# Kernel optimization log

Hardware: AMD Instinct MI355X
Metric: run time of the kernel (lower is better)

The kernel has to match this reference:

```python
import jax, jax.numpy as jnp
import numpy as np

BIG_NUMBER = 1000000.0


def setup_inputs() -> dict:
    key = jax.random.key(0)
    ks = jax.random.split(key, 20)
    B, N, F, MID, OUT = 2, 512, 128, 128, 128
    node_fts = jax.random.normal(ks[0], (B, N, F), jnp.float32)
    edge_fts = jax.random.normal(ks[1], (B, N, N, F), jnp.float32)
    graph_fts = jax.random.normal(ks[2], (B, F), jnp.float32)
    hidden = jax.random.normal(ks[3], (B, N, F), jnp.float32)
    # Bernoulli(0.5) adjacency + self-loops so masked max is always valid
    adj = (jax.random.uniform(ks[4], (B, N, N)) < 0.5).astype(jnp.float32)
    adj = jnp.maximum(adj, jnp.eye(N, dtype=jnp.float32)[None])
    Z = 2 * F  # z = cat(node_fts, hidden)

    def lin(k, fan_in, fan_out):
        kw, kb = jax.random.split(k)
        lim = 1.0 / np.sqrt(fan_in)
        W = jax.random.uniform(kw, (fan_in, fan_out), jnp.float32, -lim, lim)
        b = jax.random.uniform(kb, (fan_out,), jnp.float32, -lim, lim)
        return W, b

    W1, b1 = lin(ks[5], Z, MID)
    W2, b2 = lin(ks[6], Z, MID)
    We, be = lin(ks[7], F, MID)
    Wg, bg = lin(ks[8], F, MID)
    Wo1, bo1 = lin(ks[9], Z, OUT)
    Wo2, bo2 = lin(ks[10], MID, OUT)
    return dict(node_fts=node_fts, edge_fts=edge_fts, graph_fts=graph_fts,
                adj_mat=adj, hidden=hidden,
                W1=W1, b1=b1, W2=W2, b2=b2, We=We, be=be, Wg=Wg, bg=bg,
                Wo1=Wo1, bo1=bo1, Wo2=Wo2, bo2=bo2)


def reference(node_fts, edge_fts, graph_fts, adj_mat, hidden,
              W1, b1, W2, b2, We, be, Wg, bg, Wo1, bo1, Wo2, bo2):
    # z: (B, N, 2F)
    z = jnp.concatenate([node_fts, hidden], axis=-1)
    msg_1 = z @ W1 + b1                      # (B, N, mid) - sender
    msg_2 = z @ W2 + b2                      # (B, N, mid) - receiver
    msg_e = edge_fts @ We + be               # (B, N, N, mid)
    msg_g = graph_fts @ Wg + bg              # (B, mid)
    # msgs[b, i, j] = msg_1[b, j] + msg_2[b, i] + msg_e[b, i, j] + msg_g[b]
    msgs = (msg_1[:, None, :, :] + msg_2[:, :, None, :]
            + msg_e + msg_g[:, None, None, :])  # (B, N, N, mid)
    # masked max over axis 1 (senders in the torch reduction dim=1)
    maxarg = jnp.where(adj_mat[..., None] > 0, msgs, -BIG_NUMBER)
    msgs_red = jnp.max(maxarg, axis=1)       # (B, N, mid)
    h_1 = z @ Wo1 + bo1
    h_2 = msgs_red @ Wo2 + bo2
    ret = jax.nn.relu(h_1 + h_2)             # (B, N, out)
    return ret
```

## Files before the change

### kernel.cpp

```cpp
#include <hip/hip_runtime.h>


typedef __bf16 bf16x8 __attribute__((ext_vector_type(8)));
typedef float  f32x4  __attribute__((ext_vector_type(4)));

#define MFMA16(a,b,c) __builtin_amdgcn_mfma_f32_16x16x32_bf16(a,b,c,0,0,0)

union BFrag { bf16x8 v; unsigned short s[8]; unsigned u[4]; };

__device__ __forceinline__ unsigned packbf(float lo, float hi){
  return __builtin_amdgcn_perm(__builtin_bit_cast(unsigned, hi),
                               __builtin_bit_cast(unsigned, lo), 0x07060302u);
}
__device__ __forceinline__ unsigned short f2bt(float f){
  return (unsigned short)(__builtin_bit_cast(unsigned, f) >> 16);
}
__device__ __forceinline__ unsigned short f2b(float f){
  unsigned u = __builtin_bit_cast(unsigned, f);
  u = u + 0x7FFFu + ((u >> 16) & 1u);
  return (unsigned short)(u >> 16);
}
__device__ __forceinline__ float b2f(unsigned short u){
  unsigned v = ((unsigned)u) << 16;
  return __builtin_bit_cast(float, v);
}

#define WAITVM(N) asm volatile("s_waitcnt vmcnt(" #N ")" ::: "memory")

#define WS_MS2  0
#define WS_MS1  131072
#define WS_H1   262144
#define WS_MSGG 393216
#define WS_PART 393472
#define WS_WEFR 4587776

__global__ __launch_bounds__(64) void k1_small(
    const float* __restrict__ node,
    const float* __restrict__ hidden,
    const float* __restrict__ graph,
    const float* __restrict__ W1, const float* __restrict__ b1,
    const float* __restrict__ W2, const float* __restrict__ b2,
    const float* __restrict__ Wo1,const float* __restrict__ bo1,
    const float* __restrict__ Wg, const float* __restrict__ bg,
    const float* __restrict__ We,
    float* __restrict__ ws)
{
  int bid  = blockIdx.x;
  int lane = threadIdx.x;
  int col = lane & 15, quad = lane >> 4;

  if (bid < 192) {
    int mat = bid >> 6;
    int rt  = bid & 63;
    int r0  = rt * 16;
    const float* W  = (mat==0) ? W1 : (mat==1) ? W2 : Wo1;
    const float* bb = (mat==0) ? b1 : (mat==1) ? b2 : bo1;
    float* dst = ws + ((mat==0) ? WS_MS1 : (mat==1) ? WS_MS2 : WS_H1);

    bf16x8 a[8];
    long rowb = (long)(r0 + col) * 128;
#pragma unroll
    for (int kk = 0; kk < 8; ++kk) {
      const float* src = (kk < 4) ? node : hidden;
      int f = (kk & 3) * 32 + quad * 8;
      f32x4 v0 = *(const f32x4*)(src + rowb + f);
      f32x4 v1 = *(const f32x4*)(src + rowb + f + 4);
      BFrag t;
      t.u[0] = packbf(v0[0], v0[1]); t.u[1] = packbf(v0[2], v0[3]);
      t.u[2] = packbf(v1[0], v1[1]); t.u[3] = packbf(v1[2], v1[3]);
      a[kk] = t.v;
    }
    f32x4 acc[8];
#pragma unroll
    for (int nt = 0; nt < 8; ++nt) acc[nt] = (f32x4)0.f;
#pragma unroll
    for (int kk = 0; kk < 8; ++kk) {
      BFrag bf[8];
#pragma unroll
      for (int nt = 0; nt < 8; ++nt)
#pragma unroll
        for (int j = 0; j < 8; ++j)
          bf[nt].s[j] = f2bt(W[(kk*32 + quad*8 + j)*128 + nt*16 + col]);
#pragma unroll
      for (int nt = 0; nt < 8; ++nt) acc[nt] = MFMA16(a[kk], bf[nt].v, acc[nt]);
    }
#pragma unroll
    for (int nt = 0; nt < 8; ++nt) {
      float bv = bb[nt*16 + col];
#pragma unroll
      for (int r = 0; r < 4; ++r) {
        int row = r0 + quad*4 + r;
        dst[(long)row*128 + nt*16 + col] = acc[nt][r] + bv;
      }
    }
  } else if (bid < 194) {
    int b = bid - 192;
    float a0 = 0.f, a1 = 0.f;
    for (int k = 0; k < 128; ++k) {
      float g = graph[b*128 + k];
      a0 += g * Wg[k*128 + lane];
      a1 += g * Wg[k*128 + 64 + lane];
    }
    ws[WS_MSGG + b*128 + lane]      = a0 + bg[lane];
    ws[WS_MSGG + b*128 + 64 + lane] = a1 + bg[64 + lane];
  } else {
    unsigned short* wf = (unsigned short*)(ws + WS_WEFR);
#pragma unroll
    for (int kk = 0; kk < 4; ++kk)
#pragma unroll
      for (int nt = 0; nt < 8; ++nt) {
        BFrag t;
#pragma unroll
        for (int e = 0; e < 8; ++e)
          t.s[e] = f2b(We[(kk*32 + quad*8 + e)*128 + nt*16 + col]);
        *(bf16x8*)(wf + ((kk*8 + nt)*64 + lane)*8) = t.v;
      }
  }
}

__device__ __forceinline__ void issue_slice(const float* ei, void* lbase, int lane){
  int l5 = lane >> 5, s5 = lane & 31;
#pragma unroll
  for (int inst = 0; inst < 8; ++inst) {
    int j = inst*2 + l5;
    const float* gp = ei + j*128 + ((s5 ^ j) << 2);
    __builtin_amdgcn_global_load_lds(
        (const __attribute__((address_space(1))) void*)gp,
        (__attribute__((address_space(3))) void*)((char*)lbase + inst*1024),
        16, 0, 0);
  }
}

__global__ __launch_bounds__(64, 1) void k2_main(
    const float* __restrict__ E,
    const float* __restrict__ adj,
    const float* __restrict__ msg2,
    const unsigned short* __restrict__ wefrag,
    float* __restrict__ part)
{
  __shared__ alignas(16) unsigned char lds_raw[4*8192 + 4096 + 512];
  unsigned short* const m2l  = (unsigned short*)(lds_raw + 32768);
  unsigned short* const adjl = (unsigned short*)(lds_raw + 32768 + 4096);

  const int bid = blockIdx.x;
  const int jt = bid & 31, s = (bid >> 5) & 31, b = bid >> 10;
  const int lane = threadIdx.x;
  const int col = lane & 15, quad = lane >> 4;
  const int i0 = s * 16, j0 = jt * 16;

  const float* Eb = E + ((long)(b*512 + i0)*512 + j0) * 128;

  bf16x8 bfr[4][8];
#pragma unroll
  for (int kk = 0; kk < 4; ++kk)
#pragma unroll
    for (int nt = 0; nt < 8; ++nt)
      bfr[kk][nt] = *(const bf16x8*)(wefrag + ((kk*8 + nt)*64 + lane)*8);

#pragma unroll
  for (int p = 0; p < 8; ++p) {
    int f = p*256 + lane*4;
    const float* mp = msg2 + (long)(b*512 + i0 + (f >> 7))*128 + (f & 127);
    f32x4 v = *(const f32x4*)mp;
    uint2 uu;
    uu.x = (unsigned)f2b(v[0]) | ((unsigned)f2b(v[1]) << 16);
    uu.y = (unsigned)f2b(v[2]) | ((unsigned)f2b(v[3]) << 16);
    *(uint2*)(m2l + f) = uu;
  }
  {
    int row = lane >> 2, c4 = (lane & 3) * 4;
    f32x4 v = *(const f32x4*)(adj + (long)(b*512 + i0 + row)*512 + j0 + c4);
    uint2 uu;
    uu.x = (unsigned)f2bt(v[0]) | ((unsigned)f2bt(v[1]) << 16);
    uu.y = (unsigned)f2bt(v[2]) | ((unsigned)f2bt(v[3]) << 16);
    *(uint2*)(adjl + row*16 + c4) = uu;
  }
  __syncthreads();

#pragma unroll
  for (int d = 0; d < 4; ++d)
    issue_slice(Eb + (long)d*65536, lds_raw + d*8192, lane);

  f32x4 mx[8];
#pragma unroll
  for (int nt = 0; nt < 8; ++nt) mx[nt] = (f32x4)(-1.0e6f);

  auto body = [&](int ii) {
    const float* sl = (const float*)(lds_raw + (ii & 3) * 8192);
    BFrag a[4];
#pragma unroll
    for (int kk = 0; kk < 4; ++kk) {
      int cb = kk*8 + quad*2;
      f32x4 v0 = *(const f32x4*)(sl + col*128 + ((cb    ) ^ col)*4);
      f32x4 v1 = *(const f32x4*)(sl + col*128 + ((cb + 1) ^ col)*4);
      a[kk].u[0] = packbf(v0[0], v0[1]); a[kk].u[1] = packbf(v0[2], v0[3]);
      a[kk].u[2] = packbf(v1[0], v1[1]); a[kk].u[3] = packbf(v1[2], v1[3]);
    }
    float m2[8];
#pragma unroll
    for (int nt = 0; nt < 8; ++nt) m2[nt] = b2f(m2l[ii*128 + nt*16 + col]);
    ushort4 av = *(const ushort4*)(adjl + ii*16 + quad*4);
    f32x4 biasv;
    biasv[0] = b2f(av.x)*1.0e6f - 1.0e6f;
    biasv[1] = b2f(av.y)*1.0e6f - 1.0e6f;
    biasv[2] = b2f(av.z)*1.0e6f - 1.0e6f;
    biasv[3] = b2f(av.w)*1.0e6f - 1.0e6f;
    f32x4 T[8];
#pragma unroll
    for (int nt = 0; nt < 8; ++nt) T[nt] = biasv + m2[nt];
#pragma unroll
    for (int kk = 0; kk < 4; ++kk)
#pragma unroll
      for (int nt = 0; nt < 8; ++nt)
        T[nt] = MFMA16(a[kk].v, bfr[kk][nt], T[nt]);
#pragma unroll
    for (int nt = 0; nt < 8; ++nt)
#pragma unroll
      for (int r = 0; r < 4; ++r)
        mx[nt][r] = fmaxf(mx[nt][r], T[nt][r]);
  };

#pragma unroll 1
  for (int ii = 0; ii < 12; ++ii) {
    WAITVM(24);
    body(ii);
    asm volatile("" ::: "memory");
    issue_slice(Eb + (long)(ii+4)*65536, lds_raw + (ii & 3)*8192, lane);
  }
  WAITVM(24); body(12);
  WAITVM(16); body(13);
  WAITVM(8);  body(14);
  WAITVM(0);  body(15);

  float* pp = part + ((long)((b*32 + jt)*32 + s)) * 2048;
#pragma unroll
  for (int nt = 0; nt < 8; ++nt)
#pragma unroll
    for (int r = 0; r < 4; ++r)
      pp[(quad*4 + r)*128 + nt*16 + col] = mx[nt][r];
}

__global__ __launch_bounds__(64) void k3_out(
    const float* __restrict__ ws,
    const float* __restrict__ Wo2,
    const float* __restrict__ be,
    const float* __restrict__ bo2,
    float* __restrict__ out)
{
  int bid = blockIdx.x;
  int b = bid >> 5, jt = bid & 31, j0 = jt * 16;
  int lane = threadIdx.x, col = lane & 15, quad = lane >> 4;

  const float* part = ws + WS_PART + ((long)((b*32 + jt)*32))*2048;
  const float* msg1 = ws + WS_MS1;
  const float* msgg = ws + WS_MSGG + b*128;
  const float* h1   = ws + WS_H1;

  BFrag af[4];
#pragma unroll
  for (int kk = 0; kk < 4; ++kk) {
    int off = kk*32 + quad*8;
    const float* p0 = part + col*128 + off;
    f32x4 v0 = *(const f32x4*)(p0);
    f32x4 v1 = *(const f32x4*)(p0 + 4);
#pragma unroll
    for (int s = 1; s < 32; ++s) {
      f32x4 u0 = *(const f32x4*)(p0 + s*2048);
      f32x4 u1 = *(const f32x4*)(p0 + s*2048 + 4);
#pragma unroll
      for (int r = 0; r < 4; ++r) { v0[r] = fmaxf(v0[r], u0[r]); v1[r] = fmaxf(v1[r], u1[r]); }
    }
    const float* m1 = msg1 + (long)(b*512 + j0 + col)*128 + off;
    f32x4 w0 = *(const f32x4*)m1, w1 = *(const f32x4*)(m1 + 4);
#pragma unroll
    for (int r = 0; r < 4; ++r) {
      float g0 = msgg[off + r]     + be[off + r];
      float g1 = msgg[off + 4 + r] + be[off + 4 + r];
      af[kk].s[r]     = f2b(v0[r] + w0[r] + g0);
      af[kk].s[4 + r] = f2b(v1[r] + w1[r] + g1);
    }
  }

  f32x4 acc[8];
#pragma unroll
  for (int nt = 0; nt < 8; ++nt) acc[nt] = (f32x4)0.f;
#pragma unroll
  for (int kk = 0; kk < 4; ++kk) {
    BFrag bf[8];
#pragma unroll
    for (int nt = 0; nt < 8; ++nt)
#pragma unroll
      for (int j = 0; j < 8; ++j)
        bf[nt].s[j] = f2bt(Wo2[(kk*32 + quad*8 + j)*128 + nt*16 + col]);
#pragma unroll
    for (int nt = 0; nt < 8; ++nt) acc[nt] = MFMA16(af[kk].v, bf[nt].v, acc[nt]);
  }

#pragma unroll
  for (int nt = 0; nt < 8; ++nt) {
    float bv = bo2[nt*16 + col];
#pragma unroll
    for (int r = 0; r < 4; ++r) {
      int row = j0 + quad*4 + r;
      long idx = (long)(b*512 + row)*128 + nt*16 + col;
      float v = h1[idx] + acc[nt][r] + bv;
      out[idx] = v < 0.f ? 0.f : v;
    }
  }
}

extern "C" void kernel_launch(void* const* d_in, const int* in_sizes, int n_in,
                              void* d_out, int out_size, void* d_ws, size_t ws_size,
                              hipStream_t stream)
{
  const float* node   = (const float*)d_in[0];
  const float* E      = (const float*)d_in[1];
  const float* graph  = (const float*)d_in[2];
  const float* adj    = (const float*)d_in[3];
  const float* hidden = (const float*)d_in[4];
  const float* W1  = (const float*)d_in[5];
  const float* b1  = (const float*)d_in[6];
  const float* W2  = (const float*)d_in[7];
  const float* b2  = (const float*)d_in[8];
  const float* We  = (const float*)d_in[9];
  const float* be  = (const float*)d_in[10];
  const float* Wg  = (const float*)d_in[11];
  const float* bg  = (const float*)d_in[12];
  const float* Wo1 = (const float*)d_in[13];
  const float* bo1 = (const float*)d_in[14];
  const float* Wo2 = (const float*)d_in[15];
  const float* bo2 = (const float*)d_in[16];
  float* ws  = (float*)d_ws;
  float* out = (float*)d_out;

  hipLaunchKernelGGL(k1_small, dim3(195), dim3(64), 0, stream,
                     node, hidden, graph, W1, b1, W2, b2, Wo1, bo1, Wg, bg, We, ws);
  hipLaunchKernelGGL(k2_main, dim3(2048), dim3(64), 0, stream,
                     E, adj, ws + WS_MS2, (const unsigned short*)(ws + WS_WEFR),
                     ws + WS_PART);
  hipLaunchKernelGGL(k3_out, dim3(64), dim3(64), 0, stream,
                     ws, Wo2, be, bo2, out);
}
```

Measured before the change: 430.7 us.

## Store partial maxima as bf16, shrink edge ring to three slots, vectorize msg2 reads

The main kernel now writes its per-slice partial max results as bf16 rather than fp32, which halves the partial-buffer traffic between k2 and k3. k3 reads these partials with 16-byte bf16 loads. The prefetch ring for edge slices drops from four 8KB LDS slots to three, reducing LDS per block at the cost of less prefetch depth. msg2 is stored transposed in LDS so each lane fetches its eight values with one vector load instead of eight scalar loads. The extra bf16 rounding of the partial maxima may slightly change numerics.

```diff
diff --git a/kernel.cpp b/kernel.cpp
--- a/kernel.cpp
+++ b/kernel.cpp
@@ -136,11 +136,11 @@
     const float* __restrict__ adj,
     const float* __restrict__ msg2,
     const unsigned short* __restrict__ wefrag,
-    float* __restrict__ part)
+    unsigned short* __restrict__ part)
 {
-  __shared__ alignas(16) unsigned char lds_raw[4*8192 + 4096 + 512];
-  unsigned short* const m2l  = (unsigned short*)(lds_raw + 32768);
-  unsigned short* const adjl = (unsigned short*)(lds_raw + 32768 + 4096);
+  __shared__ alignas(16) unsigned char lds_raw[3*8192 + 4096 + 512];
+  unsigned short* const m2l  = (unsigned short*)(lds_raw + 24576);
+  unsigned short* const adjl = (unsigned short*)(lds_raw + 24576 + 4096);
 
   const int bid = blockIdx.x;
   const int jt = bid & 31, s = (bid >> 5) & 31, b = bid >> 10;
@@ -160,12 +160,13 @@
 #pragma unroll
   for (int p = 0; p < 8; ++p) {
     int f = p*256 + lane*4;
-    const float* mp = msg2 + (long)(b*512 + i0 + (f >> 7))*128 + (f & 127);
+    int i = f >> 7, c = f & 127;
+    int cc = c & 15, nt = c >> 4;
+    const float* mp = msg2 + (long)(b*512 + i0 + i)*128 + c;
     f32x4 v = *(const f32x4*)mp;
-    uint2 uu;
-    uu.x = (unsigned)f2b(v[0]) | ((unsigned)f2b(v[1]) << 16);
-    uu.y = (unsigned)f2b(v[2]) | ((unsigned)f2b(v[3]) << 16);
-    *(uint2*)(m2l + f) = uu;
+#pragma unroll
+    for (int e = 0; e < 4; ++e)
+      m2l[i*128 + (cc + e)*8 + nt] = f2b(v[e]);
   }
   {
     int row = lane >> 2, c4 = (lane & 3) * 4;
@@ -178,15 +179,15 @@
   __syncthreads();
 
 #pragma unroll
-  for (int d = 0; d < 4; ++d)
+  for (int d = 0; d < 3; ++d)
     issue_slice(Eb + (long)d*65536, lds_raw + d*8192, lane);
 
   f32x4 mx[8];
 #pragma unroll
   for (int nt = 0; nt < 8; ++nt) mx[nt] = (f32x4)(-1.0e6f);
 
-  auto body = [&](int ii) {
-    const float* sl = (const float*)(lds_raw + (ii & 3) * 8192);
+  auto body = [&](int ii, int slot) {
+    const float* sl = (const float*)(lds_raw + slot * 8192);
     BFrag a[4];
 #pragma unroll
     for (int kk = 0; kk < 4; ++kk) {
@@ -196,9 +197,8 @@
       a[kk].u[0] = packbf(v0[0], v0[1]); a[kk].u[1] = packbf(v0[2], v0[3]);
       a[kk].u[2] = packbf(v1[0], v1[1]); a[kk].u[3] = packbf(v1[2], v1[3]);
     }
-    float m2[8];
-#pragma unroll
-    for (int nt = 0; nt < 8; ++nt) m2[nt] = b2f(m2l[ii*128 + nt*16 + col]);
+    BFrag m2f;
+    m2f.v = *(const bf16x8*)(m2l + ii*128 + col*8);
     ushort4 av = *(const ushort4*)(adjl + ii*16 + quad*4);
     f32x4 biasv;
     biasv[0] = b2f(av.x)*1.0e6f - 1.0e6f;
@@ -207,7 +207,7 @@
     biasv[3] = b2f(av.w)*1.0e6f - 1.0e6f;
     f32x4 T[8];
 #pragma unroll
-    for (int nt = 0; nt < 8; ++nt) T[nt] = biasv + m2[nt];
+    for (int nt = 0; nt < 8; ++nt) T[nt] = biasv + b2f(m2f.s[nt]);
 #pragma unroll
     for (int kk = 0; kk < 4; ++kk)
 #pragma unroll
@@ -220,24 +220,25 @@
         mx[nt][r] = fmaxf(mx[nt][r], T[nt][r]);
   };
 
+  int slot = 0;
 #pragma unroll 1
-  for (int ii = 0; ii < 12; ++ii) {
-    WAITVM(24);
-    body(ii);
+  for (int ii = 0; ii < 13; ++ii) {
+    WAITVM(16);
+    body(ii, slot);
     asm volatile("" ::: "memory");
-    issue_slice(Eb + (long)(ii+4)*65536, lds_raw + (ii & 3)*8192, lane);
-  }
-  WAITVM(24); body(12);
-  WAITVM(16); body(13);
-  WAITVM(8);  body(14);
-  WAITVM(0);  body(15);
-
-  float* pp = part + ((long)((b*32 + jt)*32 + s)) * 2048;
+    issue_slice(Eb + (long)(ii+3)*65536, lds_raw + slot*8192, lane);
+    slot = (slot == 2) ? 0 : slot + 1;
+  }
+  WAITVM(16); body(13, 1);
+  WAITVM(8);  body(14, 2);
+  WAITVM(0);  body(15, 0);
+
+  unsigned short* pp = part + ((long)((b*32 + jt)*32 + s)) * 2048;
 #pragma unroll
   for (int nt = 0; nt < 8; ++nt)
 #pragma unroll
     for (int r = 0; r < 4; ++r)
-      pp[(quad*4 + r)*128 + nt*16 + col] = mx[nt][r];
+      pp[(quad*4 + r)*128 + nt*16 + col] = f2b(mx[nt][r]);
 }
 
 __global__ __launch_bounds__(64) void k3_out(
@@ -251,7 +252,8 @@
   int b = bid >> 5, jt = bid & 31, j0 = jt * 16;
   int lane = threadIdx.x, col = lane & 15, quad = lane >> 4;
 
-  const float* part = ws + WS_PART + ((long)((b*32 + jt)*32))*2048;
+  const unsigned short* part =
+      (const unsigned short*)(ws + WS_PART) + ((long)((b*32 + jt)*32))*2048;
   const float* msg1 = ws + WS_MS1;
   const float* msgg = ws + WS_MSGG + b*128;
   const float* h1   = ws + WS_H1;
@@ -260,15 +262,15 @@
 #pragma unroll
   for (int kk = 0; kk < 4; ++kk) {
     int off = kk*32 + quad*8;
-    const float* p0 = part + col*128 + off;
-    f32x4 v0 = *(const f32x4*)(p0);
-    f32x4 v1 = *(const f32x4*)(p0 + 4);
-#pragma unroll
-    for (int s = 1; s < 32; ++s) {
-      f32x4 u0 = *(const f32x4*)(p0 + s*2048);
-      f32x4 u1 = *(const f32x4*)(p0 + s*2048 + 4);
-#pragma unroll
-      for (int r = 0; r < 4; ++r) { v0[r] = fmaxf(v0[r], u0[r]); v1[r] = fmaxf(v1[r], u1[r]); }
+    const unsigned short* p0 = part + col*128 + off;
+    float v[8];
+#pragma unroll
+    for (int e = 0; e < 8; ++e) v[e] = -1.0e6f;
+#pragma unroll
+    for (int s = 0; s < 32; ++s) {
+      BFrag t; t.v = *(const bf16x8*)(p0 + s*2048);
+#pragma unroll
+      for (int e = 0; e < 8; ++e) v[e] = fmaxf(v[e], b2f(t.s[e]));
     }
     const float* m1 = msg1 + (long)(b*512 + j0 + col)*128 + off;
     f32x4 w0 = *(const f32x4*)m1, w1 = *(const f32x4*)(m1 + 4);
@@ -276,8 +278,8 @@
     for (int r = 0; r < 4; ++r) {
       float g0 = msgg[off + r]     + be[off + r];
       float g1 = msgg[off + 4 + r] + be[off + 4 + r];
-      af[kk].s[r]     = f2b(v0[r] + w0[r] + g0);
-      af[kk].s[4 + r] = f2b(v1[r] + w1[r] + g1);
+      af[kk].s[r]     = f2b(v[r]     + w0[r] + g0);
+      af[kk].s[4 + r] = f2b(v[4 + r] + w1[r] + g1);
     }
   }
 
@@ -337,7 +339,7 @@
                      node, hidden, graph, W1, b1, W2, b2, Wo1, bo1, Wg, bg, We, ws);
   hipLaunchKernelGGL(k2_main, dim3(2048), dim3(64), 0, stream,
                      E, adj, ws + WS_MS2, (const unsigned short*)(ws + WS_WEFR),
-                     ws + WS_PART);
+                     (unsigned short*)(ws + WS_PART));
   hipLaunchKernelGGL(k3_out, dim3(64), dim3(64), 0, stream,
                      ws, Wo2, be, bo2, out);
 }
```

Result: faster. 419.7 us (-2.5%).
